# Optimization experiments

Hardware: AMD Instinct MI355X
Metric: run time of the kernel (lower is better)

Reference implementation:

```python
import jax, jax.numpy as jnp
import numpy as np

N, E, D, H, C = 50000, 800000, 128, 4, 32  # nodes, edges, embed dim, heads, head dim


def setup_inputs() -> dict:
    key = jax.random.key(0)
    ks = jax.random.split(key, 9)
    s = 1.0 / np.sqrt(D)
    return {
        "edge_index": jax.random.randint(ks[0], (2, E), 0, N),
        "emb": jax.random.normal(ks[1], (N, D), dtype=jnp.float32) * s,
        "W1": jax.random.normal(ks[2], (D, H * C), dtype=jnp.float32) * s,
        "att_src1": jax.random.normal(ks[3], (H, C), dtype=jnp.float32) * s,
        "att_dst1": jax.random.normal(ks[4], (H, C), dtype=jnp.float32) * s,
        "b1": jnp.zeros((H * C,), dtype=jnp.float32),
        "W2": jax.random.normal(ks[5], (D, D), dtype=jnp.float32) * s,
        "att_src2": jax.random.normal(ks[6], (1, D), dtype=jnp.float32) * s,
        "att_dst2": jax.random.normal(ks[7], (1, D), dtype=jnp.float32) * s,
        "b2": jnp.zeros((D,), dtype=jnp.float32),
    }


def _gat_conv(x, src, dst, W, a_src, a_dst, b, concat):
    """PyG-style GATConv: edge attention logits, segment softmax over dst, scatter-add."""
    n = x.shape[0]
    h, c = a_src.shape
    xl = (x @ W).reshape(n, h, c)                    # [N,H,C]
    a_s = (xl * a_src).sum(-1)                        # [N,H]
    a_d = (xl * a_dst).sum(-1)                        # [N,H]
    logits = jax.nn.leaky_relu(a_s[src] + a_d[dst], negative_slope=0.2)  # [E2,H]
    m = jax.ops.segment_max(logits, dst, num_segments=n)                 # per-dst max
    e = jnp.exp(logits - m[dst])
    denom = jax.ops.segment_sum(e, dst, num_segments=n)
    alpha = e / (denom[dst] + 1e-16)                  # [E2,H]
    msg = xl[src] * alpha[:, :, None]                 # [E2,H,C]
    out = jax.ops.segment_sum(msg, dst, num_segments=n)  # [N,H,C]
    out = out.reshape(n, h * c) if concat else out.mean(axis=1)
    return out + b


def reference(edge_index, emb, W1, att_src1, att_dst1, b1, W2, att_src2, att_dst2, b2):
    n = emb.shape[0]
    loop = jnp.arange(n)  # GATConv default add_self_loops=True
    src = jnp.concatenate([edge_index[0], loop])
    dst = jnp.concatenate([edge_index[1], loop])
    x = _gat_conv(emb, src, dst, W1, att_src1, att_dst1, b1, True)
    x = jax.nn.elu(x)
    x = _gat_conv(x, src, dst, W2, att_src2, att_dst2, b2, False)
    return x / jnp.maximum(jnp.linalg.norm(x, axis=1, keepdims=True), 1e-12)
```

## Files before the change

kernel.cpp:

```cpp
#include <hip/hip_runtime.h>
#include <hip/hip_bf16.h>
#include <math.h>

#define DD 128
#define CAP 64
#define NBKT 256
#define BCAP 5120
#define PCHUNK 2048
#define CSUB 8

typedef __attribute__((ext_vector_type(8))) short bf16x8;
typedef __attribute__((ext_vector_type(4))) float f32x4;

__device__ __forceinline__ float lrelu02(float x){ return x > 0.f ? x : 0.2f*x; }
__device__ __forceinline__ short f2bf(float f){
  __hip_bfloat16 h = __float2bfloat16(f);
  union { __hip_bfloat16 b; short s; } u; u.b = h; return u.s;
}

__global__ __launch_bounds__(256) void k_prepW(
    const float* __restrict__ W1, short* __restrict__ Wt1,
    const float* __restrict__ W2, short* __restrict__ Wt2,
    int* __restrict__ bcnt)
{
  int idx = blockIdx.x*256 + threadIdx.x;
  if (idx < NBKT) bcnt[idx] = 0;
  if (idx < 2*DD*DD){
    const float* W = (idx < DD*DD) ? W1 : W2;
    short* Wt      = (idx < DD*DD) ? Wt1 : Wt2;
    int i2 = idx & (DD*DD - 1);
    int k = i2 >> 7, nn = i2 & 127;
    Wt[nn*DD + k] = f2bf(W[i2]);
  }
}

__global__ __launch_bounds__(256) void k_part(
    const int* __restrict__ src, const int* __restrict__ dst,
    int* __restrict__ bcnt, unsigned int* __restrict__ part, int E)
{
  __shared__ int hist[NBKT];
  __shared__ int base[NBKT];
  int e0 = blockIdx.x * PCHUNK;
  int e1 = min(e0 + PCHUNK, E);
  hist[threadIdx.x] = 0;
  __syncthreads();
  for (int e = e0 + (int)threadIdx.x; e < e1; e += 256)
    atomicAdd(&hist[dst[e] >> 8], 1);
  __syncthreads();
  {
    int h = hist[threadIdx.x];
    base[threadIdx.x] = h ? atomicAdd(&bcnt[threadIdx.x], h) : 0;
  }
  __syncthreads();
  hist[threadIdx.x] = 0;
  __syncthreads();
  for (int e = e0 + (int)threadIdx.x; e < e1; e += 256){
    int d = dst[e];
    int b = d >> 8;
    int pos = base[b] + atomicAdd(&hist[b], 1);
    if (pos < BCAP)
      part[b*BCAP + pos] = ((unsigned int)src[e] << 16) | (unsigned int)(d & 255);
  }
}

__global__ __launch_bounds__(256) void k_csr(
    const int* __restrict__ bcnt, const unsigned int* __restrict__ part,
    int* __restrict__ cnt, unsigned short* __restrict__ csr, int N)
{
  __shared__ int cur[32];
  int b   = blockIdx.x >> 3;
  int sub = blockIdx.x & (CSUB-1);
  int nb = min(bcnt[b], BCAP);
  if (threadIdx.x < 32) cur[threadIdx.x] = 0;
  __syncthreads();
  const unsigned int* pb = part + (size_t)b*BCAP;
  for (int t = threadIdx.x; t < nb; t += 256){
    unsigned int pk = pb[t];
    int j = pk & 255;
    if ((j >> 5) == sub){
      int pos = atomicAdd(&cur[j & 31], 1);
      if (pos < CAP){
        int d = (b << 8) | j;
        csr[d*CAP + pos] = (unsigned short)(pk >> 16);
      }
    }
  }
  __syncthreads();
  if (threadIdx.x < 32){
    int d = (b << 8) | (sub << 5) | (int)threadIdx.x;
    if (d < N) cnt[d] = min(cur[threadIdx.x], CAP);
  }
}

template<int MODE>
__global__ __launch_bounds__(256) void k_gemm_mfma(
    const void* __restrict__ xin, const short* __restrict__ Wt,
    const float* __restrict__ att_s, const float* __restrict__ att_d,
    short* __restrict__ xl, float* __restrict__ as_, float* __restrict__ ad_, int n)
{
  __shared__ short Wl[DD*DD];
  {
    const float4* g = (const float4*)Wt;
    for (int c = threadIdx.x; c < DD*DD/8; c += 256){
      int row = c >> 4;
      int off = (c & 15) << 4;
      *(float4*)((char*)Wl + row*256 + (off ^ ((row&7)<<4))) = g[c];
    }
  }
  __syncthreads();

  const int lane = threadIdx.x & 63;
  const int wv   = threadIdx.x >> 6;
  const int col  = lane & 15;
  const int kg   = lane >> 4;
  const int row0 = blockIdx.x * 128;

  f32x4 acc[2][8];
  #pragma unroll
  for (int m=0;m<2;++m)
    #pragma unroll
    for (int t=0;t<8;++t) acc[m][t] = (f32x4){0.f,0.f,0.f,0.f};

  #pragma unroll
  for (int ks = 0; ks < 4; ++ks){
    bf16x8 afrag[2];
    #pragma unroll
    for (int m=0;m<2;++m){
      int r = row0 + wv*32 + m*16 + col;
      if (MODE == 0){
        bf16x8 a = (bf16x8)(short)0;
        if (r < n){
          const float* xf = (const float*)xin + (size_t)r*DD + ks*32 + kg*8;
          float4 fa = *(const float4*)xf;
          float4 fb = *(const float4*)(xf+4);
          a[0]=f2bf(fa.x); a[1]=f2bf(fa.y); a[2]=f2bf(fa.z); a[3]=f2bf(fa.w);
          a[4]=f2bf(fb.x); a[5]=f2bf(fb.y); a[6]=f2bf(fb.z); a[7]=f2bf(fb.w);
        }
        afrag[m] = a;
      } else {
        const short* xb = (const short*)xin + (size_t)r*DD + ks*32 + kg*8;
        afrag[m] = (r < n) ? *(const bf16x8*)xb : (bf16x8)(short)0;
      }
    }
    #pragma unroll
    for (int nt=0; nt<8; ++nt){
      int nrow = nt*16 + col;
      int koff = ks*64 + kg*16;
      bf16x8 b = *(const bf16x8*)((const char*)Wl + nrow*256 + (koff ^ ((nrow&7)<<4)));
      acc[0][nt] = __builtin_amdgcn_mfma_f32_16x16x32_bf16(afrag[0], b, acc[0][nt], 0,0,0);
      acc[1][nt] = __builtin_amdgcn_mfma_f32_16x16x32_bf16(afrag[1], b, acc[1][nt], 0,0,0);
    }
  }

  float ats[8], atd[8];
  #pragma unroll
  for (int nt=0;nt<8;++nt){ ats[nt]=att_s[nt*16+col]; atd[nt]=att_d[nt*16+col]; }

  #pragma unroll
  for (int m=0;m<2;++m){
    #pragma unroll
    for (int j=0;j<4;++j){
      int grow = row0 + wv*32 + m*16 + kg*4 + j;
      if (MODE==0){
        float ps[4]={0,0,0,0}, pd[4]={0,0,0,0};
        #pragma unroll
        for (int nt=0;nt<8;++nt){
          ps[nt>>1] += acc[m][nt][j]*ats[nt];
          pd[nt>>1] += acc[m][nt][j]*atd[nt];
        }
        #pragma unroll
        for (int h=0;h<4;++h){
          #pragma unroll
          for (int off=8; off; off>>=1){
            ps[h] += __shfl_xor(ps[h], off, 16);
            pd[h] += __shfl_xor(pd[h], off, 16);
          }
        }
        if (col==0 && grow<n){
          #pragma unroll
          for (int h=0;h<4;++h){ as_[grow*4+h]=ps[h]; ad_[grow*4+h]=pd[h]; }
        }
      } else {
        float ps=0, pd=0;
        #pragma unroll
        for (int nt=0;nt<8;++nt){ ps += acc[m][nt][j]*ats[nt]; pd += acc[m][nt][j]*atd[nt]; }
        #pragma unroll
        for (int off=8; off; off>>=1){
          ps += __shfl_xor(ps, off, 16);
          pd += __shfl_xor(pd, off, 16);
        }
        if (col==0 && grow<n){ as_[grow]=ps; ad_[grow]=pd; }
      }
    }
  }

  __syncthreads();
  #pragma unroll
  for (int m=0;m<2;++m)
    #pragma unroll
    for (int nt=0;nt<8;++nt)
      #pragma unroll
      for (int j=0;j<4;++j){
        int rl = wv*32 + m*16 + kg*4 + j;
        Wl[rl*DD + nt*16 + col] = f2bf(acc[m][nt][j]);
      }
  __syncthreads();
  {
    int rl = threadIdx.x >> 1;
    int grow = row0 + rl;
    if (grow < n){
      const float4* s = (const float4*)((const char*)Wl + rl*256 + (threadIdx.x&1)*128);
      float4* d = (float4*)((char*)xl + (size_t)grow*256 + (threadIdx.x&1)*128);
      #pragma unroll
      for (int q=0;q<8;++q) d[q]=s[q];
    }
  }
}

template<int HMODE>
__device__ __forceinline__ void agg_body(
    const unsigned int* __restrict__ xl, const float* __restrict__ as_,
    float adh, int lane, int h, int c, int b0, int n,
    const unsigned short* __restrict__ csr,
    float& a0, float& a1, float& den)
{
  const int jl = lane & 15;
  for (int e = 0; e < c; e += 16){
    int slot = min(e + jl, c - 1);
    int sw = csr[b0 + slot];
    float logit = (HMODE == 4) ? as_[sw*4 + h] : as_[sw];
    float wl = __expf(lrelu02(logit + adh));

    uint4 pk0 = *(const uint4*)(csr + b0 + e);
    uint4 pk1 = *(const uint4*)(csr + b0 + e + 8);
    unsigned int s16[16];
    s16[0]=pk0.x&0xffffu;  s16[1]=pk0.x>>16;  s16[2]=pk0.y&0xffffu;  s16[3]=pk0.y>>16;
    s16[4]=pk0.z&0xffffu;  s16[5]=pk0.z>>16;  s16[6]=pk0.w&0xffffu;  s16[7]=pk0.w>>16;
    s16[8]=pk1.x&0xffffu;  s16[9]=pk1.x>>16;  s16[10]=pk1.y&0xffffu; s16[11]=pk1.y>>16;
    s16[12]=pk1.z&0xffffu; s16[13]=pk1.z>>16; s16[14]=pk1.w&0xffffu; s16[15]=pk1.w>>16;

    if (e + 16 <= c){
      #pragma unroll
      for (int j = 0; j < 16; ++j){
        unsigned int v = xl[(size_t)s16[j]*64 + lane];
        float wj = __shfl(wl, (lane & 48) + j, 64);
        a0 += wj * __uint_as_float(v << 16);
        a1 += wj * __uint_as_float(v & 0xffff0000u);
        den += wj;
      }
    } else {
      int rem = c - e;
      #pragma unroll
      for (int j = 0; j < 16; ++j){
        unsigned int sj = min(s16[j], (unsigned int)(n - 1));
        unsigned int v = xl[(size_t)sj*64 + lane];
        float wj = __shfl(wl, (lane & 48) + j, 64);
        wj = (j < rem) ? wj : 0.f;
        a0 += wj * __uint_as_float(v << 16);
        a1 += wj * __uint_as_float(v & 0xffff0000u);
        den += wj;
      }
    }
  }
}

__global__ __launch_bounds__(256) void k_agg1(
    const unsigned int* __restrict__ xl, const float* __restrict__ as_,
    const float* __restrict__ ad_, const int* __restrict__ cnt,
    const unsigned short* __restrict__ csr,
    const float* __restrict__ b, unsigned int* __restrict__ out, int n)
{
  int wv = threadIdx.x >> 6, lane = threadIdx.x & 63;
  int i = blockIdx.x*4 + wv;
  if (i >= n) return;
  int h = lane >> 4;
  float adh = ad_[i*4+h];
  float wslf = __expf(lrelu02(as_[i*4+h] + adh));
  unsigned int xv = xl[(size_t)i*64 + lane];
  float a0 = wslf * __uint_as_float(xv << 16);
  float a1 = wslf * __uint_as_float(xv & 0xffff0000u);
  float den = wslf;
  int b0 = i*CAP;
  int c = min(cnt[i], CAP);

  agg_body<4>(xl, as_, adh, lane, h, c, b0, n, csr, a0, a1, den);

  float inv = 1.f/(den + 1e-16f);
  float o0 = a0*inv + b[2*lane];
  float o1 = a1*inv + b[2*lane+1];
  o0 = o0 > 0.f ? o0 : (__expf(o0)-1.f);
  o1 = o1 > 0.f ? o1 : (__expf(o1)-1.f);
  unsigned int p = ((unsigned int)(unsigned short)f2bf(o1) << 16) | (unsigned int)(unsigned short)f2bf(o0);
  out[(size_t)i*64 + lane] = p;
}

__global__ __launch_bounds__(256) void k_agg2(
    const unsigned int* __restrict__ xl, const float* __restrict__ as_,
    const float* __restrict__ ad_, const int* __restrict__ cnt,
    const unsigned short* __restrict__ csr,
    const float* __restrict__ b, float* __restrict__ out, int n)
{
  int wv = threadIdx.x >> 6, lane = threadIdx.x & 63;
  int i = blockIdx.x*4 + wv;
  if (i >= n) return;
  float adh = ad_[i];
  float wslf = __expf(lrelu02(as_[i] + adh));
  unsigned int xv = xl[(size_t)i*64 + lane];
  float a0 = wslf * __uint_as_float(xv << 16);
  float a1 = wslf * __uint_as_float(xv & 0xffff0000u);
  float den = wslf;
  int b0 = i*CAP;
  int c = min(cnt[i], CAP);

  agg_body<1>(xl, as_, adh, lane, 0, c, b0, n, csr, a0, a1, den);

  float inv = 1.f/(den + 1e-16f);
  float o0 = a0*inv + b[2*lane];
  float o1 = a1*inv + b[2*lane+1];
  float sq = o0*o0 + o1*o1;
  #pragma unroll
  for (int off = 32; off; off >>= 1) sq += __shfl_xor(sq, off, 64);
  float r = 1.f / fmaxf(sqrtf(sq), 1e-12f);
  ((float2*)(out + (size_t)i*DD))[lane] = make_float2(o0*r, o1*r);
}

extern "C" void kernel_launch(void* const* d_in, const int* in_sizes, int n_in,
                              void* d_out, int out_size, void* d_ws, size_t ws_size,
                              hipStream_t stream) {
  const int*   ei   = (const int*)d_in[0];
  const float* emb  = (const float*)d_in[1];
  const float* W1   = (const float*)d_in[2];
  const float* as1w = (const float*)d_in[3];
  const float* ad1w = (const float*)d_in[4];
  const float* b1   = (const float*)d_in[5];
  const float* W2   = (const float*)d_in[6];
  const float* as2w = (const float*)d_in[7];
  const float* ad2w = (const float*)d_in[8];
  const float* b2   = (const float*)d_in[9];
  const int E = in_sizes[0] / 2;
  const int N = in_sizes[1] / DD;
  const int* srcp = ei;
  const int* dstp = ei + E;

  char* p = (char*)d_ws;
  auto alloc = [&](size_t bytes)->void*{
    void* r = (void*)p; p += (bytes + 255) & ~(size_t)255; return r;
  };
  int*            cntb = (int*)alloc((size_t)N*4);
  int*            bcnt = (int*)alloc((size_t)NBKT*4);
  unsigned int*   part = (unsigned int*)alloc((size_t)NBKT*BCAP*4);
  unsigned short* csr  = (unsigned short*)alloc((size_t)N*CAP*2);
  short* Wt1    = (short*)alloc((size_t)DD*DD*2);
  short* Wt2    = (short*)alloc((size_t)DD*DD*2);
  short* xl1    = (short*)alloc((size_t)N*DD*2);
  short* x1     = (short*)alloc((size_t)N*DD*2);
  short* xl2    = (short*)alloc((size_t)N*DD*2);
  float* as1    = (float*)alloc((size_t)N*4*4);
  float* ad1    = (float*)alloc((size_t)N*4*4);
  float* as2    = (float*)alloc((size_t)N*4);
  float* ad2    = (float*)alloc((size_t)N*4);

  int nbk = (N + 255) / 256;
  k_prepW<<<2*DD*DD/256, 256, 0, stream>>>(W1, Wt1, W2, Wt2, bcnt);
  k_part <<<(E + PCHUNK - 1)/PCHUNK, 256, 0, stream>>>(srcp, dstp, bcnt, part, E);
  k_csr  <<<nbk*CSUB, 256, 0, stream>>>(bcnt, part, cntb, csr, N);

  int gg = (N + 127) / 128;
  int gb = (N + 3) / 4;
  k_gemm_mfma<0><<<gg, 256, 0, stream>>>((const void*)emb, Wt1, as1w, ad1w, xl1, as1, ad1, N);
  k_agg1        <<<gb, 256, 0, stream>>>((const unsigned int*)xl1, as1, ad1, cntb, csr, b1, (unsigned int*)x1, N);
  k_gemm_mfma<1><<<gg, 256, 0, stream>>>((const void*)x1, Wt2, as2w, ad2w, xl2, as2, ad2, N);
  k_agg2        <<<gb, 256, 0, stream>>>((const unsigned int*)xl2, as2, ad2, cntb, csr, b2, (float*)d_out, N);
}
```

Measured before the change: 137.2 us.

## Replace atomic bucket partition with histogram, scan, and LDS-staged scatter

Edge bucketing now runs in three steps instead of one partition kernel that took global atomic offsets. A per-chunk histogram pass is fused with the weight transpose, a separate kernel scans each bucket's offsets across chunks, and a scatter kernel stages packed edges in shared memory sorted by bucket before writing them out. The aim is deterministic bucket offsets without global atomics and more contiguous writes to the partition buffer. In exchange it adds a kernel launch, reads dst twice more, stores a global histogram buffer, and doubles the chunk size, which leaves fewer blocks for the edge passes.

```diff
diff --git a/kernel.cpp b/kernel.cpp
--- a/kernel.cpp
+++ b/kernel.cpp
@@ -6,7 +6,7 @@
 #define CAP 64
 #define NBKT 256
 #define BCAP 5120
-#define PCHUNK 2048
+#define PCHUNK 4096
 #define CSUB 8
 
 typedef __attribute__((ext_vector_type(8))) short bf16x8;
@@ -18,13 +18,15 @@
   union { __hip_bfloat16 b; short s; } u; u.b = h; return u.s;
 }
 
-__global__ __launch_bounds__(256) void k_prepW(
+__global__ __launch_bounds__(256) void k_prep_hist(
     const float* __restrict__ W1, short* __restrict__ Wt1,
     const float* __restrict__ W2, short* __restrict__ Wt2,
-    int* __restrict__ bcnt)
-{
-  int idx = blockIdx.x*256 + threadIdx.x;
-  if (idx < NBKT) bcnt[idx] = 0;
+    const int* __restrict__ dst, int* __restrict__ ghist, int E)
+{
+  __shared__ int hist[NBKT];
+  int tid = threadIdx.x;
+  hist[tid] = 0;
+  int idx = blockIdx.x*256 + tid;
   if (idx < 2*DD*DD){
     const float* W = (idx < DD*DD) ? W1 : W2;
     short* Wt      = (idx < DD*DD) ? Wt1 : Wt2;
@@ -32,34 +34,87 @@
     int k = i2 >> 7, nn = i2 & 127;
     Wt[nn*DD + k] = f2bf(W[i2]);
   }
-}
-
-__global__ __launch_bounds__(256) void k_part(
-    const int* __restrict__ src, const int* __restrict__ dst,
-    int* __restrict__ bcnt, unsigned int* __restrict__ part, int E)
-{
-  __shared__ int hist[NBKT];
-  __shared__ int base[NBKT];
+  __syncthreads();
   int e0 = blockIdx.x * PCHUNK;
   int e1 = min(e0 + PCHUNK, E);
-  hist[threadIdx.x] = 0;
-  __syncthreads();
-  for (int e = e0 + (int)threadIdx.x; e < e1; e += 256)
+  for (int e = e0 + tid; e < e1; e += 256)
     atomicAdd(&hist[dst[e] >> 8], 1);
   __syncthreads();
-  {
-    int h = hist[threadIdx.x];
-    base[threadIdx.x] = h ? atomicAdd(&bcnt[threadIdx.x], h) : 0;
-  }
-  __syncthreads();
-  hist[threadIdx.x] = 0;
-  __syncthreads();
-  for (int e = e0 + (int)threadIdx.x; e < e1; e += 256){
+  if (e0 < E) ghist[blockIdx.x*NBKT + tid] = hist[tid];
+}
+
+__global__ __launch_bounds__(64) void k_scan(
+    int* __restrict__ ghist, int* __restrict__ bcnt, int nblk)
+{
+  int b = blockIdx.x;
+  int lane = threadIdx.x;
+  int running = 0;
+  for (int i0 = 0; i0 < nblk; i0 += 64){
+    int i = i0 + lane;
+    int v = (i < nblk) ? ghist[i*NBKT + b] : 0;
+    int x = v;
+    #pragma unroll
+    for (int off = 1; off < 64; off <<= 1){
+      int t = __shfl(x, lane - off, 64);
+      if (lane >= off) x += t;
+    }
+    if (i < nblk) ghist[i*NBKT + b] = running + (x - v);
+    running += __shfl(x, 63, 64);
+  }
+  if (lane == 0) bcnt[b] = running;
+}
+
+__global__ __launch_bounds__(256) void k_scatter2(
+    const int* __restrict__ src, const int* __restrict__ dst,
+    const int* __restrict__ ghist, unsigned int* __restrict__ part, int E)
+{
+  __shared__ int hist[NBKT];
+  __shared__ int lb[NBKT];
+  __shared__ int gb[NBKT];
+  __shared__ unsigned int sdata[PCHUNK];
+  __shared__ unsigned int saddr[PCHUNK];
+  int tid = threadIdx.x;
+  int e0 = blockIdx.x * PCHUNK;
+  int e1 = min(e0 + PCHUNK, E);
+  hist[tid] = 0;
+  gb[tid] = ghist[blockIdx.x*NBKT + tid];
+  __syncthreads();
+  for (int e = e0 + tid; e < e1; e += 256)
+    atomicAdd(&hist[dst[e] >> 8], 1);
+  __syncthreads();
+  if (tid < 64){
+    int s0 = hist[4*tid], s1 = hist[4*tid+1], s2 = hist[4*tid+2], s3 = hist[4*tid+3];
+    int s = s0 + s1 + s2 + s3;
+    int x = s;
+    #pragma unroll
+    for (int off = 1; off < 64; off <<= 1){
+      int t = __shfl(x, tid - off, 64);
+      if (tid >= off) x += t;
+    }
+    int base = x - s;
+    lb[4*tid]   = base;
+    lb[4*tid+1] = base + s0;
+    lb[4*tid+2] = base + s0 + s1;
+    lb[4*tid+3] = base + s0 + s1 + s2;
+  }
+  __syncthreads();
+  hist[tid] = 0;
+  __syncthreads();
+  for (int e = e0 + tid; e < e1; e += 256){
     int d = dst[e];
     int b = d >> 8;
-    int pos = base[b] + atomicAdd(&hist[b], 1);
-    if (pos < BCAP)
-      part[b*BCAP + pos] = ((unsigned int)src[e] << 16) | (unsigned int)(d & 255);
+    unsigned int pk = ((unsigned int)src[e] << 16) | (unsigned int)(d & 255);
+    int pos = atomicAdd(&hist[b], 1);
+    int loc = lb[b] + pos;
+    int off = gb[b] + pos;
+    sdata[loc] = pk;
+    saddr[loc] = (off < BCAP) ? (unsigned int)(b*BCAP + off) : 0xFFFFFFFFu;
+  }
+  __syncthreads();
+  int cn = e1 - e0;
+  for (int t = tid; t < cn; t += 256){
+    unsigned int a = saddr[t];
+    if (a != 0xFFFFFFFFu) part[a] = sdata[t];
   }
 }
 
@@ -341,15 +396,17 @@
   const int N = in_sizes[1] / DD;
   const int* srcp = ei;
   const int* dstp = ei + E;
+  const int nblk = (E + PCHUNK - 1) / PCHUNK;
 
   char* p = (char*)d_ws;
   auto alloc = [&](size_t bytes)->void*{
     void* r = (void*)p; p += (bytes + 255) & ~(size_t)255; return r;
   };
-  int*            cntb = (int*)alloc((size_t)N*4);
-  int*            bcnt = (int*)alloc((size_t)NBKT*4);
-  unsigned int*   part = (unsigned int*)alloc((size_t)NBKT*BCAP*4);
-  unsigned short* csr  = (unsigned short*)alloc((size_t)N*CAP*2);
+  int*            cntb  = (int*)alloc((size_t)N*4);
+  int*            bcnt  = (int*)alloc((size_t)NBKT*4);
+  int*            ghist = (int*)alloc((size_t)nblk*NBKT*4);
+  unsigned int*   part  = (unsigned int*)alloc((size_t)NBKT*BCAP*4);
+  unsigned short* csr   = (unsigned short*)alloc((size_t)N*CAP*2);
   short* Wt1    = (short*)alloc((size_t)DD*DD*2);
   short* Wt2    = (short*)alloc((size_t)DD*DD*2);
   short* xl1    = (short*)alloc((size_t)N*DD*2);
@@ -361,9 +418,11 @@
   float* ad2    = (float*)alloc((size_t)N*4);
 
   int nbk = (N + 255) / 256;
-  k_prepW<<<2*DD*DD/256, 256, 0, stream>>>(W1, Wt1, W2, Wt2, bcnt);
-  k_part <<<(E + PCHUNK - 1)/PCHUNK, 256, 0, stream>>>(srcp, dstp, bcnt, part, E);
-  k_csr  <<<nbk*CSUB, 256, 0, stream>>>(bcnt, part, cntb, csr, N);
+  int g1 = nblk > 2*DD*DD/256 ? nblk : 2*DD*DD/256;
+  k_prep_hist<<<g1, 256, 0, stream>>>(W1, Wt1, W2, Wt2, dstp, ghist, E);
+  k_scan     <<<NBKT, 64, 0, stream>>>(ghist, bcnt, nblk);
+  k_scatter2 <<<nblk, 256, 0, stream>>>(srcp, dstp, ghist, part, E);
+  k_csr      <<<nbk*CSUB, 256, 0, stream>>>(bcnt, part, cntb, csr, N);
 
   int gg = (N + 127) / 128;
   int gb = (N + 3) / 4;
```

Measured after the change: 137.2 us. No clear change (-0.0%).
